# Performance work log

Hardware: AMD Instinct MI355X
Metric: run time of the kernel (lower is better)

The kernel has to match this reference:

```python
import jax, jax.numpy as jnp
import numpy as np

N_USER = 60000
N_ITEM = 40000
N = N_USER + N_ITEM          # 100000 nodes
D = 64                       # embed / layer dim
NNZ = 1600000                # edges per relation (avg degree 16)
B = 16384                    # batch of (user,item) pairs
NLAYERS = 2                  # layers=[64,64,64] -> 2 GNN layers
VAL_SCALE = 0.02             # ~1/degree, mimics symmetric-normalized Laplacian values
W_SCALE = 0.05


def spmm(row, col, val, X):
    # sparse [N,N] @ dense [N,D] via gather + segment-sum (COO)
    return jax.ops.segment_sum(val[:, None] * X[col], row, num_segments=N)


def setup_inputs() -> dict:
    key = jax.random.key(0)
    ks = jax.random.split(key, 40)
    inp = {}
    inp['userIdx'] = jax.random.randint(ks[0], (B,), 0, N_USER, dtype=jnp.int32)
    inp['itemIdx'] = jax.random.randint(ks[1], (B,), 0, N_ITEM, dtype=jnp.int32)
    inp['uEmbd'] = jax.random.normal(ks[2], (N_USER, D), dtype=jnp.float32)
    inp['iEmbd'] = jax.random.normal(ks[3], (N_ITEM, D), dtype=jnp.float32)
    for i, name in enumerate(['lap', 'trust', 'add']):
        inp[name + '_row'] = jax.random.randint(ks[4 + 3 * i], (NNZ,), 0, N, dtype=jnp.int32)
        inp[name + '_col'] = jax.random.randint(ks[5 + 3 * i], (NNZ,), 0, N, dtype=jnp.int32)
        inp[name + '_val'] = jax.random.uniform(ks[6 + 3 * i], (NNZ,), dtype=jnp.float32) * VAL_SCALE
    j = 13
    for name in ['lin_W', 'inter_W', 'attM_W', 'attA_W', 'attT_W']:
        inp[name] = jax.random.normal(ks[j], (NLAYERS, D, D), dtype=jnp.float32) * W_SCALE; j += 1
    for name in ['lin_b', 'inter_b', 'attM_b', 'attA_b', 'attT_b']:
        inp[name] = jax.random.normal(ks[j], (NLAYERS, D), dtype=jnp.float32) * W_SCALE; j += 1
    for name in ['a_main', 'a_add', 'a_trust']:
        inp[name] = jax.random.normal(ks[j], (NLAYERS, D, 1), dtype=jnp.float32) * W_SCALE; j += 1
    inp['W1'] = jax.random.normal(ks[j], (2 * D, 64), dtype=jnp.float32) * W_SCALE; j += 1
    inp['b1'] = jax.random.normal(ks[j], (64,), dtype=jnp.float32) * W_SCALE; j += 1
    inp['W2'] = jax.random.normal(ks[j], (64, 32), dtype=jnp.float32) * W_SCALE; j += 1
    inp['b2'] = jax.random.normal(ks[j], (32,), dtype=jnp.float32) * W_SCALE; j += 1
    inp['W3'] = jax.random.normal(ks[j], (32, 1), dtype=jnp.float32) * W_SCALE; j += 1
    inp['b3'] = jax.random.normal(ks[j], (1,), dtype=jnp.float32) * W_SCALE; j += 1
    return inp


def _gcf_forward(userIdx, itemIdx, uEmbd, iEmbd,
                 lap_row, lap_col, lap_val,
                 trust_row, trust_col, trust_val,
                 add_row, add_col, add_val,
                 lin_W, lin_b, inter_W, inter_b,
                 attM_W, attM_b, attA_W, attA_b, attT_W, attT_b,
                 a_main, a_add, a_trust,
                 W1, b1, W2, b2, W3, b3):
    feats = jnp.concatenate([uEmbd, iEmbd], axis=0)  # [N, D]
    all_emb = [feats]
    rels = [(lap_row, lap_col, lap_val),
            (trust_row, trust_col, trust_val),
            (add_row, add_col, add_val)]
    for l in range(NLAYERS):
        X = feats
        X2 = X * X  # inter_feature = features * features

        def relation(edges, aW, ab, avec):
            row, col, val = edges
            # (L + I) @ X  -> linear ; L @ (X*X) -> interActTransform
            h1 = (spmm(row, col, val, X) + X) @ lin_W[l] + lin_b[l]
            h2 = spmm(row, col, val, X2) @ inter_W[l] + inter_b[l]
            att = jnp.tanh((h1 + h2) @ aW + ab) @ avec  # [N, 1]
            return h1, h2, att.mean()

        m1, m2, w_main = relation(rels[0], attM_W[l], attM_b[l], a_main[l])
        t1, t2, w_trust = relation(rels[1], attT_W[l], attT_b[l], a_trust[l])
        a1, a2, w_add = relation(rels[2], attA_W[l], attA_b[l], a_add[l])
        beta = jax.nn.softmax(jnp.stack([w_main, w_add, w_trust]))  # [3]
        feats = (beta[0] * (m1 + m2) + beta[1] * (a1 + a2) + beta[2] * (t1 + t2))
        all_emb.append(feats)
    final = jnp.mean(jnp.stack(all_emb, axis=1), axis=1)  # [N, D]
    userE = final[userIdx]
    itemE = final[itemIdx + N_USER]
    h = jnp.concatenate([userE, itemE], axis=1)  # [B, 2D]
    h = jax.nn.relu(h @ W1 + b1)
    h = h @ W2 + b2
    h = h @ W3 + b3
    prediction = h.reshape(-1)
    return prediction, userE, itemE, final


def reference(userIdx, itemIdx, uEmbd, iEmbd,
              lap_row, lap_col, lap_val,
              trust_row, trust_col, trust_val,
              add_row, add_col, add_val,
              lin_W, lin_b, inter_W, inter_b,
              attM_W, attM_b, attA_W, attA_b, attT_W, attT_b,
              a_main, a_add, a_trust,
              W1, b1, W2, b2, W3, b3):
    return _gcf_forward(userIdx, itemIdx, uEmbd, iEmbd,
                        lap_row, lap_col, lap_val,
                        trust_row, trust_col, trust_val,
                        add_row, add_col, add_val,
                        lin_W, lin_b, inter_W, inter_b,
                        attM_W, attM_b, attA_W, attA_b, attT_W, attT_b,
                        a_main, a_add, a_trust,
                        W1, b1, W2, b2, W3, b3)
```

## Files before the change

### kernel.cpp

```cpp
#include <hip/hip_runtime.h>

#define N_USER  60000
#define N_ITEM  40000
#define NN      100000
#define NNZ_E   1600000
#define BB      16384
#define ND      6400000
#define ND4     1600000
#define NCHUNK  6250
#define NBUCK   196
#define BUCK_CAP 9216
#define BUCKTOT (NBUCK * BUCK_CAP)
#define BINB    196
#define EPB     8192

typedef __attribute__((ext_vector_type(8))) short bf16x8;
typedef __attribute__((ext_vector_type(8))) unsigned short u16x8;
typedef __attribute__((ext_vector_type(4))) float f32x4;

__device__ __forceinline__ float tanh_fast(float x) {
    x = fminf(fmaxf(x, -15.f), 15.f);
    float e = __expf(2.f * x);
    return (e - 1.f) / (e + 1.f);
}

__device__ __forceinline__ float bcast(float x, int k) {
    return __int_as_float(__builtin_amdgcn_readlane(__float_as_int(x), k));
}

__device__ __forceinline__ unsigned short f2bf(float f) {
    unsigned u = __float_as_uint(f);
    u += 0x7FFFu + ((u >> 16) & 1u);
    return (unsigned short)(u >> 16);
}
__device__ __forceinline__ float bf2f(unsigned short s) {
    return __uint_as_float(((unsigned)s) << 16);
}

__device__ __forceinline__ int widx(int k, int n) {
    return ((((n >> 4) * 2 + (k >> 5)) * 4 + ((k >> 3) & 3)) * 16 + (n & 15)) * 8 + (k & 7);
}

__global__ __launch_bounds__(256) void init_kernel(
    const float4* __restrict__ u, const float4* __restrict__ it,
    ushort* __restrict__ XB, float4* __restrict__ fs,
    int* __restrict__ CURS, float* __restrict__ attsum)
{
    int i = blockIdx.x * 256 + threadIdx.x;
    if (i < ND4) {
        float4 v = (i < N_USER * 16) ? u[i] : it[i - N_USER * 16];
        fs[i] = v;
        ushort4 b;
        b.x = f2bf(v.x); b.y = f2bf(v.y); b.z = f2bf(v.z); b.w = f2bf(v.w);
        ((ushort4*)XB)[i] = b;
    }
    if (i < 3 * NBUCK) CURS[i] = (i % NBUCK) * BUCK_CAP;
    if (i < 6) attsum[i] = 0.f;
}

__global__ __launch_bounds__(512) void bin_kernel(
    const int* __restrict__ rows0, const int* __restrict__ cols0, const float* __restrict__ vals0,
    const int* __restrict__ rows1, const int* __restrict__ cols1, const float* __restrict__ vals1,
    const int* __restrict__ rows2, const int* __restrict__ cols2, const float* __restrict__ vals2,
    int* __restrict__ CURS, int2* __restrict__ ECV)
{
    int rel = blockIdx.x / BINB;
    int blk = blockIdx.x % BINB;
    const int* rows; const int* cols; const float* vals;
    if (rel == 0) { rows = rows0; cols = cols0; vals = vals0; }
    else if (rel == 1) { rows = rows1; cols = cols1; vals = vals1; }
    else { rows = rows2; cols = cols2; vals = vals2; }
    long long* out = (long long*)(ECV + (size_t)rel * BUCKTOT);

    __shared__ int2 sStage[EPB];
    __shared__ int hW[8 * NBUCK];
    __shared__ int lOff[NBUCK], lEnd[NBUCK], lCur[NBUCK], gB[NBUCK];
    __shared__ int wt[4];

    int t = threadIdx.x;
    int lane = t & 63, w = t >> 6;
    for (int i = t; i < 8 * NBUCK; i += 512) hW[i] = 0;
    __syncthreads();

    int base = blk * EPB;
    int myrow[16];
    #pragma unroll
    for (int j = 0; j < 16; ++j) {
        int idx = base + j * 512 + t;
        myrow[j] = (idx < NNZ_E) ? __builtin_nontemporal_load(&rows[idx]) : -1;
        if (myrow[j] >= 0) atomicAdd(&hW[w * NBUCK + (myrow[j] >> 9)], 1);
    }
    __syncthreads();
    if (t < 256) {
        int h = 0;
        if (t < NBUCK) {
            #pragma unroll
            for (int ww = 0; ww < 8; ++ww) h += hW[ww * NBUCK + t];
        }
        int sc = h;
        #pragma unroll
        for (int o = 1; o < 64; o <<= 1) {
            int u = __shfl_up(sc, o);
            if (lane >= o) sc += u;
        }
        if (lane == 63) wt[w] = sc;
        __syncthreads();
        int woff = 0;
        #pragma unroll
        for (int ww = 0; ww < 4; ++ww) if (ww < w) woff += wt[ww];
        int excl = woff + sc - h;
        if (t < NBUCK) {
            lOff[t] = excl;
            lEnd[t] = excl + h;
            lCur[t] = excl;
            gB[t] = h ? atomicAdd(&CURS[rel * NBUCK + t], h) : 0;
        }
    } else {
        __syncthreads();
    }
    __syncthreads();
    #pragma unroll
    for (int j = 0; j < 16; ++j) {
        int idx = base + j * 512 + t;
        if (myrow[j] >= 0) {
            int c = __builtin_nontemporal_load(&cols[idx]);
            float v = __builtin_nontemporal_load(&vals[idx]);
            int b = myrow[j] >> 9;
            int pos = atomicAdd(&lCur[b], 1);
            int2 e;
            e.x = ((myrow[j] & 511) << 17) | c;
            e.y = __float_as_int(v);
            sStage[pos] = e;
        }
    }
    __syncthreads();
    for (int b = w; b < NBUCK; b += 8) {
        int s = lOff[b], e = lEnd[b];
        int gb = gB[b];
        int lim = (b + 1) * BUCK_CAP;
        for (int i = s + lane; i < e; i += 64) {
            int d = gb + (i - s);
            if (d < lim) {
                int2 ev = sStage[i];
                long long packed = (((long long)(unsigned)ev.y) << 32) | (unsigned)ev.x;
                __builtin_nontemporal_store(packed, &out[d]);
            }
        }
    }
}

__global__ __launch_bounds__(512) void bsort_kernel(
    const int* __restrict__ CURS, int2* __restrict__ ECV,
    int* __restrict__ RPS, int* __restrict__ RPE)
{
    int rel = blockIdx.x / NBUCK;
    int b   = blockIdx.x % NBUCK;
    int start = b * BUCK_CAP;
    int cnt = CURS[rel * NBUCK + b] - start;
    if (cnt > BUCK_CAP) cnt = BUCK_CAP;
    int2* ecv = ECV + (size_t)rel * BUCKTOT;

    __shared__ int2 sStage[BUCK_CAP];
    __shared__ int sOff[512], sCnt[512];
    __shared__ int wt[8];
    int t = threadIdx.x;
    int lane = t & 63, w = t >> 6;
    sCnt[t] = 0;
    __syncthreads();
    int2 e[18];
    #pragma unroll
    for (int j = 0; j < 18; ++j) {
        int i = t + j * 512;
        if (i < cnt) {
            e[j] = ecv[start + i];
            atomicAdd(&sCnt[((unsigned)e[j].x) >> 17], 1);
        }
    }
    __syncthreads();
    int h = sCnt[t];
    int sc = h;
    #pragma unroll
    for (int o = 1; o < 64; o <<= 1) {
        int u = __shfl_up(sc, o);
        if (lane >= o) sc += u;
    }
    if (lane == 63) wt[w] = sc;
    __syncthreads();
    int woff = 0;
    #pragma unroll
    for (int ww = 0; ww < 8; ++ww) if (ww < w) woff += wt[ww];
    int excl = woff + sc - h;
    __syncthreads();
    sOff[t] = excl;
    sCnt[t] = excl;
    __syncthreads();
    #pragma unroll
    for (int j = 0; j < 18; ++j) {
        int i = t + j * 512;
        if (i < cnt) {
            int rl = ((unsigned)e[j].x) >> 17;
            int pos = atomicAdd(&sCnt[rl], 1);
            int2 o2; o2.x = e[j].x & 0x1FFFF; o2.y = e[j].y;
            sStage[pos] = o2;
        }
    }
    __syncthreads();
    for (int i = t; i < cnt; i += 512) ecv[start + i] = sStage[i];
    int row = b * 512 + t;
    if (row < NN) {
        RPS[rel * NN + row] = start + sOff[t];
        RPE[rel * NN + row] = start + sCnt[t];
    }
}

__global__ __launch_bounds__(256, 4) void spmm_kernel(
    const int* __restrict__ RPS, const int* __restrict__ RPE,
    const int2* __restrict__ ecv,
    const ushort* __restrict__ XB, ushort* __restrict__ G)
{
    int t = threadIdx.x;
    int lane = t & 63;
    int wv = t >> 6;
    int dl = lane & 7;
    int r = blockIdx.x * 32 + wv * 8 + (lane >> 3);
    int ea = RPS[r], eb = RPE[r];
    int cnt = eb - ea;
    int cm = cnt;
    cm = max(cm, __shfl_xor(cm, 8));
    cm = max(cm, __shfl_xor(cm, 16));
    cm = max(cm, __shfl_xor(cm, 32));
    u16x8 xo8 = *(const u16x8*)&XB[(size_t)r * 64 + 8 * dl];
    float s1[8] = {0.f, 0.f, 0.f, 0.f, 0.f, 0.f, 0.f, 0.f};
    float s2[8] = {0.f, 0.f, 0.f, 0.f, 0.f, 0.f, 0.f, 0.f};
    for (int base = 0; base < cm; base += 4) {
        float vv[4]; u16x8 xx[4];
        #pragma unroll
        for (int j = 0; j < 4; ++j) {
            int i = base + j;
            bool ok = i < cnt;
            int is = ea + (ok ? i : 0);
            int2 cv = ecv[is];
            vv[j] = ok ? __int_as_float(cv.y) : 0.f;
            xx[j] = *(const u16x8*)&XB[(size_t)cv.x * 64 + 8 * dl];
        }
        #pragma unroll
        for (int j = 0; j < 4; ++j) {
            float v = vv[j];
            #pragma unroll
            for (int d = 0; d < 8; ++d) {
                float x = bf2f(xx[j][d]);
                s1[d] += v * x;
                s2[d] += v * x * x;
            }
        }
    }
    u16x8 o1, o2;
    #pragma unroll
    for (int d = 0; d < 8; ++d) {
        o1[d] = f2bf(s1[d] + bf2f(xo8[d]));
        o2[d] = f2bf(s2[d]);
    }
    *(u16x8*)&G[(size_t)r * 128 + 8 * dl]      = o1;
    *(u16x8*)&G[(size_t)r * 128 + 64 + 8 * dl] = o2;
}

__global__ __launch_bounds__(256) void dense_kernel(
    const ushort* __restrict__ G, ushort* __restrict__ Hout,
    const float* __restrict__ linW, const float* __restrict__ interW,
    const float* __restrict__ linb, const float* __restrict__ interb,
    const float* __restrict__ attW, const float* __restrict__ attb,
    const float* __restrict__ avec, float* __restrict__ attsum)
{
    __shared__ short sL[4096], sI[4096], sW[4096];
    __shared__ float sH[4 * 16 * 65];
    __shared__ float sBias[64], sAttb[64], sAvec[64];

    int tid = threadIdx.x;
    for (int i = tid; i < 4096; i += 256) {
        int k = i >> 6, n = i & 63, ix = widx(k, n);
        sL[ix] = (short)f2bf(linW[i]);
        sI[ix] = (short)f2bf(interW[i]);
        sW[ix] = (short)f2bf(attW[i]);
    }
    if (tid < 64) {
        sBias[tid] = linb[tid] + interb[tid];
        sAttb[tid] = attb[tid];
        sAvec[tid] = avec[tid];
    }
    __syncthreads();

    const bf16x8* pL = (const bf16x8*)sL;
    const bf16x8* pI = (const bf16x8*)sI;
    const bf16x8* pW = (const bf16x8*)sW;

    int lane = tid & 63;
    int wv = tid >> 6;
    int nl = lane & 15;
    int q  = lane >> 4;
    float* myH = sH + wv * (16 * 65);
    int gw = blockIdx.x * 4 + wv;
    int nw = gridDim.x * 4;
    float att_acc = 0.f;

    for (int c = gw; c < NCHUNK; c += nw) {
        int r0 = c * 16;
        const bf16x8* gp = (const bf16x8*)(G + (size_t)(r0 + nl) * 128);
        bf16x8 Ah[2], Qh[2];
        Ah[0] = gp[q];         Ah[1] = gp[4 + q];
        Qh[0] = gp[8 + q];     Qh[1] = gp[12 + q];
        #pragma unroll
        for (int nt = 0; nt < 4; ++nt) {
            float b = sBias[nt * 16 + nl];
            f32x4 acc = {b, b, b, b};
            #pragma unroll
            for (int kh = 0; kh < 2; ++kh) {
                int f = ((nt * 2 + kh) * 4 + q) * 16 + nl;
                acc = __builtin_amdgcn_mfma_f32_16x16x32_bf16(Ah[kh], pL[f], acc, 0, 0, 0);
                acc = __builtin_amdgcn_mfma_f32_16x16x32_bf16(Qh[kh], pI[f], acc, 0, 0, 0);
            }
            #pragma unroll
            for (int reg = 0; reg < 4; ++reg) {
                int row = q * 4 + reg;
                Hout[(size_t)(r0 + row) * 64 + nt * 16 + nl] = f2bf(acc[reg]);
                myH[row * 65 + nt * 16 + nl] = acc[reg];
            }
        }
        bf16x8 Th[2];
        #pragma unroll
        for (int kh = 0; kh < 2; ++kh) {
            #pragma unroll
            for (int j = 0; j < 8; ++j)
                Th[kh][j] = (short)f2bf(myH[nl * 65 + kh * 32 + q * 8 + j]);
        }
        #pragma unroll
        for (int nt = 0; nt < 4; ++nt) {
            float b = sAttb[nt * 16 + nl];
            f32x4 acc = {b, b, b, b};
            #pragma unroll
            for (int kh = 0; kh < 2; ++kh) {
                int f = ((nt * 2 + kh) * 4 + q) * 16 + nl;
                acc = __builtin_amdgcn_mfma_f32_16x16x32_bf16(Th[kh], pW[f], acc, 0, 0, 0);
            }
            float av = sAvec[nt * 16 + nl];
            #pragma unroll
            for (int reg = 0; reg < 4; ++reg)
                att_acc += tanh_fast(acc[reg]) * av;
        }
    }
    #pragma unroll
    for (int o = 32; o >= 1; o >>= 1) att_acc += __shfl_xor(att_acc, o);
    if (lane == 0) atomicAdd(attsum, att_acc);
}

__global__ __launch_bounds__(256) void combine_kernel(
    const ushort4* __restrict__ hM, const ushort4* __restrict__ hA,
    const ushort4* __restrict__ hT, const float* __restrict__ attsum,
    ushort4* __restrict__ XB, float4* __restrict__ fs, float scale)
{
    float w0 = attsum[0] * (1.f / NN);
    float w1 = attsum[1] * (1.f / NN);
    float w2 = attsum[2] * (1.f / NN);
    float m = fmaxf(w0, fmaxf(w1, w2));
    float e0 = __expf(w0 - m), e1 = __expf(w1 - m), e2 = __expf(w2 - m);
    float inv = 1.f / (e0 + e1 + e2);
    float b0 = e0 * inv, b1 = e1 * inv, b2 = e2 * inv;

    int i = blockIdx.x * 256 + threadIdx.x;
    if (i >= ND4) return;
    ushort4 um = hM[i], ua = hA[i], ut = hT[i];
    float4 x;
    x.x = b0 * bf2f(um.x) + b1 * bf2f(ua.x) + b2 * bf2f(ut.x);
    x.y = b0 * bf2f(um.y) + b1 * bf2f(ua.y) + b2 * bf2f(ut.y);
    x.z = b0 * bf2f(um.z) + b1 * bf2f(ua.z) + b2 * bf2f(ut.z);
    x.w = b0 * bf2f(um.w) + b1 * bf2f(ua.w) + b2 * bf2f(ut.w);
    ushort4 bo;
    bo.x = f2bf(x.x); bo.y = f2bf(x.y); bo.z = f2bf(x.z); bo.w = f2bf(x.w);
    XB[i] = bo;
    float4 f = fs[i];
    f.x = (f.x + x.x) * scale;
    f.y = (f.y + x.y) * scale;
    f.z = (f.z + x.z) * scale;
    f.w = (f.w + x.w) * scale;
    fs[i] = f;
}

__global__ __launch_bounds__(256) void mlp_kernel(
    const int* __restrict__ userIdx, const int* __restrict__ itemIdx,
    const float* __restrict__ fin,
    const float* __restrict__ W1, const float* __restrict__ b1,
    const float* __restrict__ W2, const float* __restrict__ b2,
    const float* __restrict__ W3, const float* __restrict__ b3,
    float* __restrict__ pred, float* __restrict__ userE, float* __restrict__ itemE)
{
    __shared__ float sW1[128 * 64];
    __shared__ float sW2[64 * 32];
    __shared__ float sW3[32];
    __shared__ float sb1[64];
    __shared__ float sb2[32];
    int tid = threadIdx.x;
    for (int i = tid; i < 8192; i += 256) sW1[i] = W1[i];
    for (int i = tid; i < 2048; i += 256) sW2[i] = W2[i];
    if (tid < 32) sW3[tid] = W3[tid];
    if (tid < 64) sb1[tid] = b1[tid];
    if (tid < 32) sb2[tid] = b2[tid];
    __syncthreads();
    float bb3 = b3[0];

    int lane = tid & 63;
    int gw = blockIdx.x * 4 + (tid >> 6);
    int nw = gridDim.x * 4;
    for (int p = gw; p < BB; p += nw) {
        int u = userIdx[p];
        int it = itemIdx[p] + N_USER;
        float ue = fin[u * 64 + lane];
        float ie = fin[it * 64 + lane];
        userE[p * 64 + lane] = ue;
        itemE[p * 64 + lane] = ie;
        float h = sb1[lane];
        #pragma unroll
        for (int k = 0; k < 64; ++k) h = fmaf(bcast(ue, k), sW1[k * 64 + lane], h);
        #pragma unroll
        for (int k = 0; k < 64; ++k) h = fmaf(bcast(ie, k), sW1[(k + 64) * 64 + lane], h);
        h = fmaxf(h, 0.f);
        float h2 = sb2[lane & 31];
        #pragma unroll
        for (int k = 0; k < 64; ++k) h2 = fmaf(bcast(h, k), sW2[k * 32 + (lane & 31)], h2);
        float c = (lane < 32) ? h2 * sW3[lane] : 0.f;
        #pragma unroll
        for (int o = 32; o >= 1; o >>= 1) c += __shfl_xor(c, o);
        if (lane == 0) pred[p] = c + bb3;
    }
}

extern "C" void kernel_launch(void* const* d_in, const int* in_sizes, int n_in,
                              void* d_out, int out_size, void* d_ws, size_t ws_size,
                              hipStream_t stream)
{
    const int*   userIdx = (const int*)d_in[0];
    const int*   itemIdx = (const int*)d_in[1];
    const float* uEmbd   = (const float*)d_in[2];
    const float* iEmbd   = (const float*)d_in[3];
    const int*   e_row[3] = {(const int*)d_in[4],  (const int*)d_in[10], (const int*)d_in[7]};
    const int*   e_col[3] = {(const int*)d_in[5],  (const int*)d_in[11], (const int*)d_in[8]};
    const float* e_val[3] = {(const float*)d_in[6], (const float*)d_in[12], (const float*)d_in[9]};
    const float* lin_W   = (const float*)d_in[13];
    const float* inter_W = (const float*)d_in[14];
    const float* attM_W  = (const float*)d_in[15];
    const float* attA_W  = (const float*)d_in[16];
    const float* attT_W  = (const float*)d_in[17];
    const float* lin_b   = (const float*)d_in[18];
    const float* inter_b = (const float*)d_in[19];
    const float* attM_b  = (const float*)d_in[20];
    const float* attA_b  = (const float*)d_in[21];
    const float* attT_b  = (const float*)d_in[22];
    const float* a_main  = (const float*)d_in[23];
    const float* a_add   = (const float*)d_in[24];
    const float* a_trust = (const float*)d_in[25];
    const float* W1 = (const float*)d_in[26];
    const float* b1 = (const float*)d_in[27];
    const float* W2 = (const float*)d_in[28];
    const float* b2 = (const float*)d_in[29];
    const float* W3 = (const float*)d_in[30];
    const float* b3 = (const float*)d_in[31];

    const float* attWq[3] = {attM_W, attA_W, attT_W};
    const float* attbq[3] = {attM_b, attA_b, attT_b};
    const float* avecq[3] = {a_main, a_add, a_trust};

    ushort* G  = (ushort*)d_ws;
    ushort* H0 = G + (size_t)NN * 128;
    ushort* H1 = H0 + ND;
    ushort* H2 = H1 + ND;
    int2*   ECV = (int2*)(H2 + ND);
    ushort* XB = (ushort*)(ECV + 3 * (size_t)BUCKTOT);
    int*    RPS = (int*)(XB + ND);
    int*    RPE = RPS + 3 * NN;
    int*    CURS = RPE + 3 * NN;
    float*  ATT = (float*)(CURS + 3 * NBUCK);

    ushort* Hs[3] = {H0, H1, H2};

    float* outPred  = (float*)d_out;
    float* outUser  = outPred + BB;
    float* outItem  = outUser + BB * 64;
    float* outFinal = outItem + BB * 64;

    init_kernel<<<6250, 256, 0, stream>>>((const float4*)uEmbd, (const float4*)iEmbd,
                                          XB, (float4*)outFinal, CURS, ATT);
    bin_kernel<<<3 * BINB, 512, 0, stream>>>(
        e_row[0], e_col[0], e_val[0],
        e_row[1], e_col[1], e_val[1],
        e_row[2], e_col[2], e_val[2], CURS, ECV);
    bsort_kernel<<<3 * NBUCK, 512, 0, stream>>>(CURS, ECV, RPS, RPE);

    for (int l = 0; l < 2; ++l) {
        const float* lw = lin_W + l * 4096;
        const float* iw = inter_W + l * 4096;
        const float* lb = lin_b + l * 64;
        const float* ib = inter_b + l * 64;

        for (int q = 0; q < 3; ++q) {
            spmm_kernel<<<3125, 256, 0, stream>>>(
                RPS + q * NN, RPE + q * NN, ECV + (size_t)q * BUCKTOT, XB, G);
            dense_kernel<<<512, 256, 0, stream>>>(
                G, Hs[q], lw, iw, lb, ib,
                attWq[q] + l * 4096, attbq[q] + l * 64, avecq[q] + l * 64,
                ATT + l * 3 + q);
        }
        combine_kernel<<<6250, 256, 0, stream>>>(
            (const ushort4*)Hs[0], (const ushort4*)Hs[1], (const ushort4*)Hs[2],
            ATT + l * 3, (ushort4*)XB, (float4*)outFinal,
            (l == 1) ? (1.f / 3.f) : 1.f);
    }

    mlp_kernel<<<512, 256, 0, stream>>>(userIdx, itemIdx, outFinal,
                                        W1, b1, W2, b2, W3, b3,
                                        outPred, outUser, outItem);
}
```

Before: 781.7 us.

## Fuse SpMM with dense MFMA attention and batch all three relations per launch

Merges the per-relation sparse aggregation and dense linear/attention kernels into one kernel. Each block aggregates 32 rows, places the bf16 results in shared memory in MFMA fragment layout, and runs the linear and attention MFMAs there, so the G intermediate no longer makes a round trip through global memory. All three relations go into a single launch, and weights are pre-converted to bf16 fragment layout once by a small prep kernel. The attention partial sums are reduced per block before one atomic add. The cost is lower occupancy (launch bounds 3), extra block-level syncs, and weight fragments read from global or L2 instead of LDS.

Result: slower. 1.024 ms (+31.0%).

```diff
diff --git a/kernel.cpp b/kernel.cpp
--- a/kernel.cpp
+++ b/kernel.cpp
@@ -7,7 +7,7 @@
 #define BB      16384
 #define ND      6400000
 #define ND4     1600000
-#define NCHUNK  6250
+#define NBLK    3125
 #define NBUCK   196
 #define BUCK_CAP 9216
 #define BUCKTOT (NBUCK * BUCK_CAP)
@@ -56,6 +56,27 @@
     }
     if (i < 3 * NBUCK) CURS[i] = (i % NBUCK) * BUCK_CAP;
     if (i < 6) attsum[i] = 0.f;
+}
+
+__global__ __launch_bounds__(256) void prep_kernel(
+    const float* __restrict__ lin_W, const float* __restrict__ inter_W,
+    const float* __restrict__ attM_W, const float* __restrict__ attA_W,
+    const float* __restrict__ attT_W, ushort* __restrict__ WF)
+{
+    int b = blockIdx.x;
+    int l = b / 5, m = b % 5;
+    const float* src;
+    if (m == 0) src = lin_W;
+    else if (m == 1) src = inter_W;
+    else if (m == 2) src = attM_W;
+    else if (m == 3) src = attA_W;
+    else src = attT_W;
+    src += (size_t)l * 4096;
+    ushort* dst = WF + ((size_t)l * 5 + m) * 4096;
+    for (int i = threadIdx.x; i < 4096; i += 256) {
+        int k = i >> 6, n = i & 63;
+        dst[widx(k, n)] = f2bf(src[i]);
+    }
 }
 
 __global__ __launch_bounds__(512) void bin_kernel(
@@ -213,22 +234,47 @@
     }
 }
 
-__global__ __launch_bounds__(256, 4) void spmm_kernel(
+__global__ __launch_bounds__(256, 3) void fused_kernel(
     const int* __restrict__ RPS, const int* __restrict__ RPE,
-    const int2* __restrict__ ecv,
-    const ushort* __restrict__ XB, ushort* __restrict__ G)
-{
+    const int2* __restrict__ ECV, const ushort* __restrict__ XB,
+    const ushort* __restrict__ WF,
+    const float* __restrict__ linb, const float* __restrict__ interb,
+    const float* __restrict__ attb0, const float* __restrict__ attb1,
+    const float* __restrict__ attb2,
+    const float* __restrict__ avec0, const float* __restrict__ avec1,
+    const float* __restrict__ avec2,
+    ushort* __restrict__ H0, ushort* __restrict__ H1, ushort* __restrict__ H2,
+    float* __restrict__ ATTl)
+{
+    __shared__ ushort sA[2048], sQ[2048];
+    __shared__ float  sH[2 * 16 * 68];
+    __shared__ float  sBias[64], sAttb[64], sAvec[64];
+    __shared__ float  sRed[4];
+
+    int bid = blockIdx.x;
+    int rel = bid / NBLK;
+    int rb  = bid % NBLK;
     int t = threadIdx.x;
-    int lane = t & 63;
-    int wv = t >> 6;
-    int dl = lane & 7;
-    int r = blockIdx.x * 32 + wv * 8 + (lane >> 3);
-    int ea = RPS[r], eb = RPE[r];
+    int lane = t & 63, wv = t >> 6, dl = lane & 7;
+
+    const float* attb = (rel == 0) ? attb0 : ((rel == 1) ? attb1 : attb2);
+    const float* avec = (rel == 0) ? avec0 : ((rel == 1) ? avec1 : avec2);
+    ushort* Hout = (rel == 0) ? H0 : ((rel == 1) ? H1 : H2);
+    if (t < 64) {
+        sBias[t] = linb[t] + interb[t];
+        sAttb[t] = attb[t];
+        sAvec[t] = avec[t];
+    }
+
+    int rr = wv * 8 + (lane >> 3);
+    int r  = rb * 32 + rr;
+    int ea = RPS[rel * NN + r], eb = RPE[rel * NN + r];
     int cnt = eb - ea;
     int cm = cnt;
     cm = max(cm, __shfl_xor(cm, 8));
     cm = max(cm, __shfl_xor(cm, 16));
     cm = max(cm, __shfl_xor(cm, 32));
+    const int2* ecv = ECV + (size_t)rel * BUCKTOT;
     u16x8 xo8 = *(const u16x8*)&XB[(size_t)r * 64 + 8 * dl];
     float s1[8] = {0.f, 0.f, 0.f, 0.f, 0.f, 0.f, 0.f, 0.f};
     float s2[8] = {0.f, 0.f, 0.f, 0.f, 0.f, 0.f, 0.f, 0.f};
@@ -254,102 +300,93 @@
             }
         }
     }
-    u16x8 o1, o2;
-    #pragma unroll
-    for (int d = 0; d < 8; ++d) {
-        o1[d] = f2bf(s1[d] + bf2f(xo8[d]));
-        o2[d] = f2bf(s2[d]);
-    }
-    *(u16x8*)&G[(size_t)r * 128 + 8 * dl]      = o1;
-    *(u16x8*)&G[(size_t)r * 128 + 64 + 8 * dl] = o2;
-}
-
-__global__ __launch_bounds__(256) void dense_kernel(
-    const ushort* __restrict__ G, ushort* __restrict__ Hout,
-    const float* __restrict__ linW, const float* __restrict__ interW,
-    const float* __restrict__ linb, const float* __restrict__ interb,
-    const float* __restrict__ attW, const float* __restrict__ attb,
-    const float* __restrict__ avec, float* __restrict__ attsum)
-{
-    __shared__ short sL[4096], sI[4096], sW[4096];
-    __shared__ float sH[4 * 16 * 65];
-    __shared__ float sBias[64], sAttb[64], sAvec[64];
-
-    int tid = threadIdx.x;
-    for (int i = tid; i < 4096; i += 256) {
-        int k = i >> 6, n = i & 63, ix = widx(k, n);
-        sL[ix] = (short)f2bf(linW[i]);
-        sI[ix] = (short)f2bf(interW[i]);
-        sW[ix] = (short)f2bf(attW[i]);
-    }
-    if (tid < 64) {
-        sBias[tid] = linb[tid] + interb[tid];
-        sAttb[tid] = attb[tid];
-        sAvec[tid] = avec[tid];
-    }
-    __syncthreads();
-
-    const bf16x8* pL = (const bf16x8*)sL;
-    const bf16x8* pI = (const bf16x8*)sI;
-    const bf16x8* pW = (const bf16x8*)sW;
-
-    int lane = tid & 63;
-    int wv = tid >> 6;
+    {
+        int ch = rr >> 4, nl15 = rr & 15, kh = dl >> 2, q4 = dl & 3;
+        int fi = ((((ch * 2 + kh) * 4 + q4) * 16) + nl15) * 8;
+        u16x8 o1, o2;
+        #pragma unroll
+        for (int d = 0; d < 8; ++d) {
+            o1[d] = f2bf(s1[d] + bf2f(xo8[d]));
+            o2[d] = f2bf(s2[d]);
+        }
+        *(u16x8*)&sA[fi] = o1;
+        *(u16x8*)&sQ[fi] = o2;
+    }
+    __syncthreads();
+
+    const bf16x8* pA = (const bf16x8*)sA;
+    const bf16x8* pQ = (const bf16x8*)sQ;
+    const bf16x8* pL = (const bf16x8*)WF;
+    const bf16x8* pI = (const bf16x8*)(WF + 4096);
+    const bf16x8* pW = (const bf16x8*)(WF + (size_t)(2 + rel) * 4096);
     int nl = lane & 15;
     int q  = lane >> 4;
-    float* myH = sH + wv * (16 * 65);
-    int gw = blockIdx.x * 4 + wv;
-    int nw = gridDim.x * 4;
+    int dch = wv >> 1;
+    int nth = wv & 1;
+    float* myH = sH + dch * (16 * 68);
+
+    bf16x8 Ah[2], Qh[2];
+    #pragma unroll
+    for (int kh = 0; kh < 2; ++kh) {
+        int f = ((dch * 2 + kh) * 4 + q) * 16 + nl;
+        Ah[kh] = pA[f];
+        Qh[kh] = pQ[f];
+    }
+    #pragma unroll
+    for (int ni = 0; ni < 2; ++ni) {
+        int nt = nth * 2 + ni;
+        float b = sBias[nt * 16 + nl];
+        f32x4 acc = {b, b, b, b};
+        #pragma unroll
+        for (int kh = 0; kh < 2; ++kh) {
+            int f = ((nt * 2 + kh) * 4 + q) * 16 + nl;
+            acc = __builtin_amdgcn_mfma_f32_16x16x32_bf16(Ah[kh], pL[f], acc, 0, 0, 0);
+            acc = __builtin_amdgcn_mfma_f32_16x16x32_bf16(Qh[kh], pI[f], acc, 0, 0, 0);
+        }
+        #pragma unroll
+        for (int reg = 0; reg < 4; ++reg)
+            myH[(q * 4 + reg) * 68 + nt * 16 + nl] = acc[reg];
+    }
+    __syncthreads();
+
+    {
+        int row = t >> 3;
+        int c0  = (t & 7) * 8;
+        const float* hp = sH + (row >> 4) * (16 * 68) + (row & 15) * 68 + c0;
+        u16x8 hv;
+        #pragma unroll
+        for (int j = 0; j < 8; ++j) hv[j] = f2bf(hp[j]);
+        *(u16x8*)&Hout[(size_t)rb * 2048 + t * 8] = hv;
+    }
+
+    bf16x8 Th[2];
+    #pragma unroll
+    for (int kh = 0; kh < 2; ++kh) {
+        #pragma unroll
+        for (int j = 0; j < 8; ++j)
+            Th[kh][j] = (short)f2bf(myH[nl * 68 + kh * 32 + q * 8 + j]);
+    }
     float att_acc = 0.f;
-
-    for (int c = gw; c < NCHUNK; c += nw) {
-        int r0 = c * 16;
-        const bf16x8* gp = (const bf16x8*)(G + (size_t)(r0 + nl) * 128);
-        bf16x8 Ah[2], Qh[2];
-        Ah[0] = gp[q];         Ah[1] = gp[4 + q];
-        Qh[0] = gp[8 + q];     Qh[1] = gp[12 + q];
-        #pragma unroll
-        for (int nt = 0; nt < 4; ++nt) {
-            float b = sBias[nt * 16 + nl];
-            f32x4 acc = {b, b, b, b};
-            #pragma unroll
-            for (int kh = 0; kh < 2; ++kh) {
-                int f = ((nt * 2 + kh) * 4 + q) * 16 + nl;
-                acc = __builtin_amdgcn_mfma_f32_16x16x32_bf16(Ah[kh], pL[f], acc, 0, 0, 0);
-                acc = __builtin_amdgcn_mfma_f32_16x16x32_bf16(Qh[kh], pI[f], acc, 0, 0, 0);
-            }
-            #pragma unroll
-            for (int reg = 0; reg < 4; ++reg) {
-                int row = q * 4 + reg;
-                Hout[(size_t)(r0 + row) * 64 + nt * 16 + nl] = f2bf(acc[reg]);
-                myH[row * 65 + nt * 16 + nl] = acc[reg];
-            }
-        }
-        bf16x8 Th[2];
+    #pragma unroll
+    for (int ni = 0; ni < 2; ++ni) {
+        int nt = nth * 2 + ni;
+        float b = sAttb[nt * 16 + nl];
+        f32x4 acc = {b, b, b, b};
         #pragma unroll
         for (int kh = 0; kh < 2; ++kh) {
-            #pragma unroll
-            for (int j = 0; j < 8; ++j)
-                Th[kh][j] = (short)f2bf(myH[nl * 65 + kh * 32 + q * 8 + j]);
-        }
-        #pragma unroll
-        for (int nt = 0; nt < 4; ++nt) {
-            float b = sAttb[nt * 16 + nl];
-            f32x4 acc = {b, b, b, b};
-            #pragma unroll
-            for (int kh = 0; kh < 2; ++kh) {
-                int f = ((nt * 2 + kh) * 4 + q) * 16 + nl;
-                acc = __builtin_amdgcn_mfma_f32_16x16x32_bf16(Th[kh], pW[f], acc, 0, 0, 0);
-            }
-            float av = sAvec[nt * 16 + nl];
-            #pragma unroll
-            for (int reg = 0; reg < 4; ++reg)
-                att_acc += tanh_fast(acc[reg]) * av;
-        }
+            int f = ((nt * 2 + kh) * 4 + q) * 16 + nl;
+            acc = __builtin_amdgcn_mfma_f32_16x16x32_bf16(Th[kh], pW[f], acc, 0, 0, 0);
+        }
+        float av = sAvec[nt * 16 + nl];
+        #pragma unroll
+        for (int reg = 0; reg < 4; ++reg)
+            att_acc += tanh_fast(acc[reg]) * av;
     }
     #pragma unroll
     for (int o = 32; o >= 1; o >>= 1) att_acc += __shfl_xor(att_acc, o);
-    if (lane == 0) atomicAdd(attsum, att_acc);
+    if (lane == 0) sRed[wv] = att_acc;
+    __syncthreads();
+    if (t == 0) atomicAdd(ATTl + rel, sRed[0] + sRed[1] + sRed[2] + sRed[3]);
 }
 
 __global__ __launch_bounds__(256) void combine_kernel(
@@ -463,12 +500,7 @@
     const float* W3 = (const float*)d_in[30];
     const float* b3 = (const float*)d_in[31];
 
-    const float* attWq[3] = {attM_W, attA_W, attT_W};
-    const float* attbq[3] = {attM_b, attA_b, attT_b};
-    const float* avecq[3] = {a_main, a_add, a_trust};
-
-    ushort* G  = (ushort*)d_ws;
-    ushort* H0 = G + (size_t)NN * 128;
+    ushort* H0 = (ushort*)d_ws;
     ushort* H1 = H0 + ND;
     ushort* H2 = H1 + ND;
     int2*   ECV = (int2*)(H2 + ND);
@@ -477,6 +509,7 @@
     int*    RPE = RPS + 3 * NN;
     int*    CURS = RPE + 3 * NN;
     float*  ATT = (float*)(CURS + 3 * NBUCK);
+    ushort* WF  = (ushort*)(ATT + 16);
 
     ushort* Hs[3] = {H0, H1, H2};
 
@@ -487,6 +520,7 @@
 
     init_kernel<<<6250, 256, 0, stream>>>((const float4*)uEmbd, (const float4*)iEmbd,
                                           XB, (float4*)outFinal, CURS, ATT);
+    prep_kernel<<<10, 256, 0, stream>>>(lin_W, inter_W, attM_W, attA_W, attT_W, WF);
     bin_kernel<<<3 * BINB, 512, 0, stream>>>(
         e_row[0], e_col[0], e_val[0],
         e_row[1], e_col[1], e_val[1],
@@ -494,19 +528,13 @@
     bsort_kernel<<<3 * NBUCK, 512, 0, stream>>>(CURS, ECV, RPS, RPE);
 
     for (int l = 0; l < 2; ++l) {
-        const float* lw = lin_W + l * 4096;
-        const float* iw = inter_W + l * 4096;
-        const float* lb = lin_b + l * 64;
-        const float* ib = inter_b + l * 64;
-
-        for (int q = 0; q < 3; ++q) {
-            spmm_kernel<<<3125, 256, 0, stream>>>(
-                RPS + q * NN, RPE + q * NN, ECV + (size_t)q * BUCKTOT, XB, G);
-            dense_kernel<<<512, 256, 0, stream>>>(
-                G, Hs[q], lw, iw, lb, ib,
-                attWq[q] + l * 4096, attbq[q] + l * 64, avecq[q] + l * 64,
-                ATT + l * 3 + q);
-        }
+        fused_kernel<<<3 * NBLK, 256, 0, stream>>>(
+            RPS, RPE, ECV, XB,
+            WF + (size_t)l * 5 * 4096,
+            lin_b + l * 64, inter_b + l * 64,
+            attM_b + l * 64, attA_b + l * 64, attT_b + l * 64,
+            a_main + l * 64, a_add + l * 64, a_trust + l * 64,
+            H0, H1, H2, ATT + l * 3);
         combine_kernel<<<6250, 256, 0, stream>>>(
             (const ushort4*)Hs[0], (const ushort4*)Hs[1], (const ushort4*)Hs[2],
             ATT + l * 3, (ushort4*)XB, (float4*)outFinal,
```

## Overlap SpMM and dense stages across relations with fused launches and double-buffered G

Applied to the files above, without the earlier changes.

Merges the init pass into the binning kernel and moves the attention-weight bf16 conversion into a small prep kernel that writes into scratch space in the output buffer. When workspace allows, G is double-buffered so each relation's dense stage runs in the same launch as the next relation's SpMM, using a block-index split. This removes serialization between dependent stages and some launch gaps. It also skips the XB write on the last combine, uses nontemporal loads there, and raises the dense grid size. The risks are the workspace-size check, the extra G buffer, and using the userE output region as temporary weight storage before mlp overwrites it.

Result: slower. 937.4 us (+19.9%).

```diff
diff --git a/kernel.cpp b/kernel.cpp
--- a/kernel.cpp
+++ b/kernel.cpp
@@ -13,6 +13,8 @@
 #define BUCKTOT (NBUCK * BUCK_CAP)
 #define BINB    196
 #define EPB     8192
+#define DGRID   1024
+#define DBLK    512
 
 typedef __attribute__((ext_vector_type(8))) short bf16x8;
 typedef __attribute__((ext_vector_type(8))) unsigned short u16x8;
@@ -41,29 +43,52 @@
     return ((((n >> 4) * 2 + (k >> 5)) * 4 + ((k >> 3) & 3)) * 16 + (n & 15)) * 8 + (k & 7);
 }
 
-__global__ __launch_bounds__(256) void init_kernel(
-    const float4* __restrict__ u, const float4* __restrict__ it,
-    ushort* __restrict__ XB, float4* __restrict__ fs,
+__global__ __launch_bounds__(256) void prep_kernel(
+    const float* __restrict__ attM_W, const float* __restrict__ attA_W,
+    const float* __restrict__ attT_W, ushort* __restrict__ WF,
     int* __restrict__ CURS, float* __restrict__ attsum)
 {
-    int i = blockIdx.x * 256 + threadIdx.x;
-    if (i < ND4) {
-        float4 v = (i < N_USER * 16) ? u[i] : it[i - N_USER * 16];
-        fs[i] = v;
-        ushort4 b;
-        b.x = f2bf(v.x); b.y = f2bf(v.y); b.z = f2bf(v.z); b.w = f2bf(v.w);
-        ((ushort4*)XB)[i] = b;
-    }
-    if (i < 3 * NBUCK) CURS[i] = (i % NBUCK) * BUCK_CAP;
-    if (i < 6) attsum[i] = 0.f;
-}
-
-__global__ __launch_bounds__(512) void bin_kernel(
+    int b = blockIdx.x;
+    if (b == 6) {
+        for (int i = threadIdx.x; i < 3 * NBUCK; i += 256)
+            CURS[i] = (i % NBUCK) * BUCK_CAP;
+        if (threadIdx.x < 16) attsum[threadIdx.x] = 0.f;
+        return;
+    }
+    int l = b / 3, q = b % 3;
+    const float* src = ((q == 0) ? attM_W : ((q == 1) ? attA_W : attT_W)) + (size_t)l * 4096;
+    ushort* dst = WF + ((size_t)l * 3 + q) * 4096;
+    for (int i = threadIdx.x; i < 4096; i += 256) {
+        int k = i >> 6, n = i & 63;
+        dst[widx(k, n)] = f2bf(src[i]);
+    }
+}
+
+__global__ __launch_bounds__(512) void ib_kernel(
     const int* __restrict__ rows0, const int* __restrict__ cols0, const float* __restrict__ vals0,
     const int* __restrict__ rows1, const int* __restrict__ cols1, const float* __restrict__ vals1,
     const int* __restrict__ rows2, const int* __restrict__ cols2, const float* __restrict__ vals2,
-    int* __restrict__ CURS, int2* __restrict__ ECV)
-{
+    int* __restrict__ CURS, int2* __restrict__ ECV,
+    const float4* __restrict__ u, const float4* __restrict__ it,
+    ushort* __restrict__ XB, float4* __restrict__ fs)
+{
+    __shared__ int2 sStage[EPB];
+    __shared__ int hW[8 * NBUCK];
+    __shared__ int lOff[NBUCK], lEnd[NBUCK], lCur[NBUCK], gB[NBUCK];
+    __shared__ int wt[4];
+
+    if (blockIdx.x >= 3 * BINB) {
+        int i = (blockIdx.x - 3 * BINB) * 512 + threadIdx.x;
+        if (i < ND4) {
+            float4 v = (i < N_USER * 16) ? u[i] : it[i - N_USER * 16];
+            fs[i] = v;
+            ushort4 b;
+            b.x = f2bf(v.x); b.y = f2bf(v.y); b.z = f2bf(v.z); b.w = f2bf(v.w);
+            ((ushort4*)XB)[i] = b;
+        }
+        return;
+    }
+
     int rel = blockIdx.x / BINB;
     int blk = blockIdx.x % BINB;
     const int* rows; const int* cols; const float* vals;
@@ -72,11 +97,6 @@
     else { rows = rows2; cols = cols2; vals = vals2; }
     long long* out = (long long*)(ECV + (size_t)rel * BUCKTOT);
 
-    __shared__ int2 sStage[EPB];
-    __shared__ int hW[8 * NBUCK];
-    __shared__ int lOff[NBUCK], lEnd[NBUCK], lCur[NBUCK], gB[NBUCK];
-    __shared__ int wt[4];
-
     int t = threadIdx.x;
     int lane = t & 63, w = t >> 6;
     for (int i = t; i < 8 * NBUCK; i += 512) hW[i] = 0;
@@ -100,8 +120,8 @@
         int sc = h;
         #pragma unroll
         for (int o = 1; o < 64; o <<= 1) {
-            int u = __shfl_up(sc, o);
-            if (lane >= o) sc += u;
+            int u2 = __shfl_up(sc, o);
+            if (lane >= o) sc += u2;
         }
         if (lane == 63) wt[w] = sc;
         __syncthreads();
@@ -213,16 +233,16 @@
     }
 }
 
-__global__ __launch_bounds__(256, 4) void spmm_kernel(
+__device__ __forceinline__ void spmm_body(
+    int t, int bid,
     const int* __restrict__ RPS, const int* __restrict__ RPE,
-    const int2* __restrict__ ecv,
-    const ushort* __restrict__ XB, ushort* __restrict__ G)
-{
-    int t = threadIdx.x;
+    const int2* __restrict__ ecv, const ushort* __restrict__ XB,
+    ushort* __restrict__ G)
+{
     int lane = t & 63;
     int wv = t >> 6;
     int dl = lane & 7;
-    int r = blockIdx.x * 32 + wv * 8 + (lane >> 3);
+    int r = bid * 32 + wv * 8 + (lane >> 3);
     int ea = RPS[r], eb = RPE[r];
     int cnt = eb - ea;
     int cm = cnt;
@@ -264,23 +284,20 @@
     *(u16x8*)&G[(size_t)r * 128 + 64 + 8 * dl] = o2;
 }
 
-__global__ __launch_bounds__(256) void dense_kernel(
+__device__ __forceinline__ void dense_body(
+    int tid, int bid, int nblk,
     const ushort* __restrict__ G, ushort* __restrict__ Hout,
     const float* __restrict__ linW, const float* __restrict__ interW,
     const float* __restrict__ linb, const float* __restrict__ interb,
-    const float* __restrict__ attW, const float* __restrict__ attb,
-    const float* __restrict__ avec, float* __restrict__ attsum)
-{
-    __shared__ short sL[4096], sI[4096], sW[4096];
-    __shared__ float sH[4 * 16 * 65];
-    __shared__ float sBias[64], sAttb[64], sAvec[64];
-
-    int tid = threadIdx.x;
+    const ushort* __restrict__ WA, const float* __restrict__ attb,
+    const float* __restrict__ avec, float* __restrict__ attsum,
+    short* sL, short* sI, float* sH,
+    float* sBias, float* sAttb, float* sAvec)
+{
     for (int i = tid; i < 4096; i += 256) {
         int k = i >> 6, n = i & 63, ix = widx(k, n);
         sL[ix] = (short)f2bf(linW[i]);
         sI[ix] = (short)f2bf(interW[i]);
-        sW[ix] = (short)f2bf(attW[i]);
     }
     if (tid < 64) {
         sBias[tid] = linb[tid] + interb[tid];
@@ -291,15 +308,15 @@
 
     const bf16x8* pL = (const bf16x8*)sL;
     const bf16x8* pI = (const bf16x8*)sI;
-    const bf16x8* pW = (const bf16x8*)sW;
+    const bf16x8* pW = (const bf16x8*)WA;
 
     int lane = tid & 63;
     int wv = tid >> 6;
     int nl = lane & 15;
     int q  = lane >> 4;
     float* myH = sH + wv * (16 * 65);
-    int gw = blockIdx.x * 4 + wv;
-    int nw = gridDim.x * 4;
+    int gw = bid * 4 + wv;
+    int nw = nblk * 4;
     float att_acc = 0.f;
 
     for (int c = gw; c < NCHUNK; c += nw) {
@@ -352,10 +369,57 @@
     if (lane == 0) atomicAdd(attsum, att_acc);
 }
 
+__global__ __launch_bounds__(256, 4) void spmm_kernel(
+    const int* __restrict__ RPS, const int* __restrict__ RPE,
+    const int2* __restrict__ ecv,
+    const ushort* __restrict__ XB, ushort* __restrict__ G)
+{
+    spmm_body(threadIdx.x, blockIdx.x, RPS, RPE, ecv, XB, G);
+}
+
+__global__ __launch_bounds__(256, 4) void dense_kernel(
+    const ushort* __restrict__ G, ushort* __restrict__ Hout,
+    const float* __restrict__ linW, const float* __restrict__ interW,
+    const float* __restrict__ linb, const float* __restrict__ interb,
+    const ushort* __restrict__ WA, const float* __restrict__ attb,
+    const float* __restrict__ avec, float* __restrict__ attsum)
+{
+    __shared__ short sL[4096], sI[4096];
+    __shared__ float sH[4 * 16 * 65];
+    __shared__ float sBias[64], sAttb[64], sAvec[64];
+    dense_body(threadIdx.x, blockIdx.x, gridDim.x, G, Hout,
+               linW, interW, linb, interb, WA, attb, avec, attsum,
+               sL, sI, sH, sBias, sAttb, sAvec);
+}
+
+__global__ __launch_bounds__(256, 4) void sd_kernel(
+    const ushort* __restrict__ Gin, ushort* __restrict__ Hout,
+    const float* __restrict__ linW, const float* __restrict__ interW,
+    const float* __restrict__ linb, const float* __restrict__ interb,
+    const ushort* __restrict__ WA, const float* __restrict__ attb,
+    const float* __restrict__ avec, float* __restrict__ attsum,
+    const int* __restrict__ RPS, const int* __restrict__ RPE,
+    const int2* __restrict__ ecv, const ushort* __restrict__ XB,
+    ushort* __restrict__ Gout)
+{
+    __shared__ short sL[4096], sI[4096];
+    __shared__ float sH[4 * 16 * 65];
+    __shared__ float sBias[64], sAttb[64], sAvec[64];
+    if (blockIdx.x < DBLK) {
+        dense_body(threadIdx.x, blockIdx.x, DBLK, Gin, Hout,
+                   linW, interW, linb, interb, WA, attb, avec, attsum,
+                   sL, sI, sH, sBias, sAttb, sAvec);
+    } else {
+        spmm_body(threadIdx.x, blockIdx.x - DBLK, RPS, RPE, ecv, XB, Gout);
+    }
+}
+
 __global__ __launch_bounds__(256) void combine_kernel(
-    const ushort4* __restrict__ hM, const ushort4* __restrict__ hA,
-    const ushort4* __restrict__ hT, const float* __restrict__ attsum,
-    ushort4* __restrict__ XB, float4* __restrict__ fs, float scale)
+    const unsigned long long* __restrict__ hM,
+    const unsigned long long* __restrict__ hA,
+    const unsigned long long* __restrict__ hT,
+    const float* __restrict__ attsum,
+    ushort4* __restrict__ XB, float4* __restrict__ fs, float scale, int doXB)
 {
     float w0 = attsum[0] * (1.f / NN);
     float w1 = attsum[1] * (1.f / NN);
@@ -367,15 +431,19 @@
 
     int i = blockIdx.x * 256 + threadIdx.x;
     if (i >= ND4) return;
-    ushort4 um = hM[i], ua = hA[i], ut = hT[i];
+    unsigned long long pm = __builtin_nontemporal_load(&hM[i]);
+    unsigned long long pa = __builtin_nontemporal_load(&hA[i]);
+    unsigned long long pt = __builtin_nontemporal_load(&hT[i]);
     float4 x;
-    x.x = b0 * bf2f(um.x) + b1 * bf2f(ua.x) + b2 * bf2f(ut.x);
-    x.y = b0 * bf2f(um.y) + b1 * bf2f(ua.y) + b2 * bf2f(ut.y);
-    x.z = b0 * bf2f(um.z) + b1 * bf2f(ua.z) + b2 * bf2f(ut.z);
-    x.w = b0 * bf2f(um.w) + b1 * bf2f(ua.w) + b2 * bf2f(ut.w);
-    ushort4 bo;
-    bo.x = f2bf(x.x); bo.y = f2bf(x.y); bo.z = f2bf(x.z); bo.w = f2bf(x.w);
-    XB[i] = bo;
+    x.x = b0 * bf2f((unsigned short)pm)         + b1 * bf2f((unsigned short)pa)         + b2 * bf2f((unsigned short)pt);
+    x.y = b0 * bf2f((unsigned short)(pm >> 16)) + b1 * bf2f((unsigned short)(pa >> 16)) + b2 * bf2f((unsigned short)(pt >> 16));
+    x.z = b0 * bf2f((unsigned short)(pm >> 32)) + b1 * bf2f((unsigned short)(pa >> 32)) + b2 * bf2f((unsigned short)(pt >> 32));
+    x.w = b0 * bf2f((unsigned short)(pm >> 48)) + b1 * bf2f((unsigned short)(pa >> 48)) + b2 * bf2f((unsigned short)(pt >> 48));
+    if (doXB) {
+        ushort4 bo;
+        bo.x = f2bf(x.x); bo.y = f2bf(x.y); bo.z = f2bf(x.z); bo.w = f2bf(x.w);
+        XB[i] = bo;
+    }
     float4 f = fs[i];
     f.x = (f.x + x.x) * scale;
     f.y = (f.y + x.y) * scale;
@@ -463,12 +531,17 @@
     const float* W3 = (const float*)d_in[30];
     const float* b3 = (const float*)d_in[31];
 
-    const float* attWq[3] = {attM_W, attA_W, attT_W};
     const float* attbq[3] = {attM_b, attA_b, attT_b};
     const float* avecq[3] = {a_main, a_add, a_trust};
 
-    ushort* G  = (ushort*)d_ws;
-    ushort* H0 = G + (size_t)NN * 128;
+    size_t gwords = (size_t)NN * 128;
+    size_t need_big = 2 * gwords * 2 + (size_t)3 * ND * 2 + (size_t)3 * BUCKTOT * 8
+                    + (size_t)ND * 2 + (size_t)6 * NN * 4 + (size_t)3 * NBUCK * 4 + 64;
+    bool big = ws_size >= need_big;
+
+    ushort* GA = (ushort*)d_ws;
+    ushort* GB = big ? (GA + gwords) : GA;
+    ushort* H0 = GB + gwords;
     ushort* H1 = H0 + ND;
     ushort* H2 = H1 + ND;
     int2*   ECV = (int2*)(H2 + ND);
@@ -485,12 +558,14 @@
     float* outItem  = outUser + BB * 64;
     float* outFinal = outItem + BB * 64;
 
-    init_kernel<<<6250, 256, 0, stream>>>((const float4*)uEmbd, (const float4*)iEmbd,
-                                          XB, (float4*)outFinal, CURS, ATT);
-    bin_kernel<<<3 * BINB, 512, 0, stream>>>(
+    ushort* WF = (ushort*)outUser;
+
+    prep_kernel<<<7, 256, 0, stream>>>(attM_W, attA_W, attT_W, WF, CURS, ATT);
+    ib_kernel<<<3 * BINB + 3125, 512, 0, stream>>>(
         e_row[0], e_col[0], e_val[0],
         e_row[1], e_col[1], e_val[1],
-        e_row[2], e_col[2], e_val[2], CURS, ECV);
+        e_row[2], e_col[2], e_val[2], CURS, ECV,
+        (const float4*)uEmbd, (const float4*)iEmbd, XB, (float4*)outFinal);
     bsort_kernel<<<3 * NBUCK, 512, 0, stream>>>(CURS, ECV, RPS, RPE);
 
     for (int l = 0; l < 2; ++l) {
@@ -499,18 +574,38 @@
         const float* lb = lin_b + l * 64;
         const float* ib = inter_b + l * 64;
 
-        for (int q = 0; q < 3; ++q) {
+        if (big) {
             spmm_kernel<<<3125, 256, 0, stream>>>(
-                RPS + q * NN, RPE + q * NN, ECV + (size_t)q * BUCKTOT, XB, G);
-            dense_kernel<<<512, 256, 0, stream>>>(
-                G, Hs[q], lw, iw, lb, ib,
-                attWq[q] + l * 4096, attbq[q] + l * 64, avecq[q] + l * 64,
-                ATT + l * 3 + q);
+                RPS, RPE, ECV, XB, GA);
+            sd_kernel<<<DBLK + 3125, 256, 0, stream>>>(
+                GA, Hs[0], lw, iw, lb, ib,
+                WF + ((size_t)l * 3 + 0) * 4096, attbq[0] + l * 64, avecq[0] + l * 64,
+                ATT + l * 3 + 0,
+                RPS + NN, RPE + NN, ECV + (size_t)BUCKTOT, XB, GB);
+            sd_kernel<<<DBLK + 3125, 256, 0, stream>>>(
+                GB, Hs[1], lw, iw, lb, ib,
+                WF + ((size_t)l * 3 + 1) * 4096, attbq[1] + l * 64, avecq[1] + l * 64,
+                ATT + l * 3 + 1,
+                RPS + 2 * NN, RPE + 2 * NN, ECV + 2 * (size_t)BUCKTOT, XB, GA);
+            dense_kernel<<<DGRID, 256, 0, stream>>>(
+                GA, Hs[2], lw, iw, lb, ib,
+                WF + ((size_t)l * 3 + 2) * 4096, attbq[2] + l * 64, avecq[2] + l * 64,
+                ATT + l * 3 + 2);
+        } else {
+            for (int q = 0; q < 3; ++q) {
+                spmm_kernel<<<3125, 256, 0, stream>>>(
+                    RPS + q * NN, RPE + q * NN, ECV + (size_t)q * BUCKTOT, XB, GA);
+                dense_kernel<<<DGRID, 256, 0, stream>>>(
+                    GA, Hs[q], lw, iw, lb, ib,
+                    WF + ((size_t)l * 3 + q) * 4096, attbq[q] + l * 64, avecq[q] + l * 64,
+                    ATT + l * 3 + q);
+            }
         }
         combine_kernel<<<6250, 256, 0, stream>>>(
-            (const ushort4*)Hs[0], (const ushort4*)Hs[1], (const ushort4*)Hs[2],
+            (const unsigned long long*)Hs[0], (const unsigned long long*)Hs[1],
+            (const unsigned long long*)Hs[2],
             ATT + l * 3, (ushort4*)XB, (float4*)outFinal,
-            (l == 1) ? (1.f / 3.f) : 1.f);
+            (l == 1) ? (1.f / 3.f) : 1.f, (l == 0) ? 1 : 0);
     }
 
     mlp_kernel<<<512, 256, 0, stream>>>(userIdx, itemIdx, outFinal,
```

## Degree-sort rows within buckets for SpMM balance; skip final XB write

Applied to the files above, without the earlier changes.

The bucket sort kernel now builds a per-bucket permutation of rows ordered by their edge count. The SpMM kernel reads its row index through this permutation, so the 8 rows sharing a wavefront have similar degrees and less time is lost to the max-degree loop bound. The combine kernel also uses nontemporal 64-bit loads and skips writing the bf16 XB buffer on the last layer, where nothing reads it. The cost is an extra indirection load per row, and output rows are written in a scattered order.

After: 819.6 us. +4.8%, slower.

```diff
diff --git a/kernel.cpp b/kernel.cpp
--- a/kernel.cpp
+++ b/kernel.cpp
@@ -151,7 +151,7 @@
 
 __global__ __launch_bounds__(512) void bsort_kernel(
     const int* __restrict__ CURS, int2* __restrict__ ECV,
-    int* __restrict__ RPS, int* __restrict__ RPE)
+    int* __restrict__ RPS, int* __restrict__ RPE, int* __restrict__ PERM)
 {
     int rel = blockIdx.x / NBUCK;
     int b   = blockIdx.x % NBUCK;
@@ -163,6 +163,7 @@
     __shared__ int2 sStage[BUCK_CAP];
     __shared__ int sOff[512], sCnt[512];
     __shared__ int wt[8];
+    __shared__ int dh[64];
     int t = threadIdx.x;
     int lane = t & 63, w = t >> 6;
     sCnt[t] = 0;
@@ -178,6 +179,7 @@
     }
     __syncthreads();
     int h = sCnt[t];
+    int myCnt = h;
     int sc = h;
     #pragma unroll
     for (int o = 1; o < 64; o <<= 1) {
@@ -211,18 +213,39 @@
         RPS[rel * NN + row] = start + sOff[t];
         RPE[rel * NN + row] = start + sCnt[t];
     }
+
+    int dbin = (row < NN) ? min(myCnt, 62) : 63;
+    if (t < 64) dh[t] = 0;
+    __syncthreads();
+    atomicAdd(&dh[dbin], 1);
+    __syncthreads();
+    if (t < 64) {
+        int v = dh[t];
+        int sc2 = v;
+        #pragma unroll
+        for (int o = 1; o < 64; o <<= 1) {
+            int u2 = __shfl_up(sc2, o);
+            if (t >= o) sc2 += u2;
+        }
+        dh[t] = sc2 - v;
+    }
+    __syncthreads();
+    int pos = atomicAdd(&dh[dbin], 1);
+    int slot = b * 512 + pos;
+    if (row < NN && slot < NN) PERM[rel * NN + slot] = row;
 }
 
 __global__ __launch_bounds__(256, 4) void spmm_kernel(
     const int* __restrict__ RPS, const int* __restrict__ RPE,
-    const int2* __restrict__ ecv,
+    const int2* __restrict__ ecv, const int* __restrict__ PERM,
     const ushort* __restrict__ XB, ushort* __restrict__ G)
 {
     int t = threadIdx.x;
     int lane = t & 63;
     int wv = t >> 6;
     int dl = lane & 7;
-    int r = blockIdx.x * 32 + wv * 8 + (lane >> 3);
+    int g = blockIdx.x * 32 + wv * 8 + (lane >> 3);
+    int r = PERM[g];
     int ea = RPS[r], eb = RPE[r];
     int cnt = eb - ea;
     int cm = cnt;
@@ -353,9 +376,11 @@
 }
 
 __global__ __launch_bounds__(256) void combine_kernel(
-    const ushort4* __restrict__ hM, const ushort4* __restrict__ hA,
-    const ushort4* __restrict__ hT, const float* __restrict__ attsum,
-    ushort4* __restrict__ XB, float4* __restrict__ fs, float scale)
+    const unsigned long long* __restrict__ hM,
+    const unsigned long long* __restrict__ hA,
+    const unsigned long long* __restrict__ hT,
+    const float* __restrict__ attsum,
+    ushort4* __restrict__ XB, float4* __restrict__ fs, float scale, int doXB)
 {
     float w0 = attsum[0] * (1.f / NN);
     float w1 = attsum[1] * (1.f / NN);
@@ -367,15 +392,19 @@
 
     int i = blockIdx.x * 256 + threadIdx.x;
     if (i >= ND4) return;
-    ushort4 um = hM[i], ua = hA[i], ut = hT[i];
+    unsigned long long pm = __builtin_nontemporal_load(&hM[i]);
+    unsigned long long pa = __builtin_nontemporal_load(&hA[i]);
+    unsigned long long pt = __builtin_nontemporal_load(&hT[i]);
     float4 x;
-    x.x = b0 * bf2f(um.x) + b1 * bf2f(ua.x) + b2 * bf2f(ut.x);
-    x.y = b0 * bf2f(um.y) + b1 * bf2f(ua.y) + b2 * bf2f(ut.y);
-    x.z = b0 * bf2f(um.z) + b1 * bf2f(ua.z) + b2 * bf2f(ut.z);
-    x.w = b0 * bf2f(um.w) + b1 * bf2f(ua.w) + b2 * bf2f(ut.w);
-    ushort4 bo;
-    bo.x = f2bf(x.x); bo.y = f2bf(x.y); bo.z = f2bf(x.z); bo.w = f2bf(x.w);
-    XB[i] = bo;
+    x.x = b0 * bf2f((unsigned short)pm)         + b1 * bf2f((unsigned short)pa)         + b2 * bf2f((unsigned short)pt);
+    x.y = b0 * bf2f((unsigned short)(pm >> 16)) + b1 * bf2f((unsigned short)(pa >> 16)) + b2 * bf2f((unsigned short)(pt >> 16));
+    x.z = b0 * bf2f((unsigned short)(pm >> 32)) + b1 * bf2f((unsigned short)(pa >> 32)) + b2 * bf2f((unsigned short)(pt >> 32));
+    x.w = b0 * bf2f((unsigned short)(pm >> 48)) + b1 * bf2f((unsigned short)(pa >> 48)) + b2 * bf2f((unsigned short)(pt >> 48));
+    if (doXB) {
+        ushort4 bo;
+        bo.x = f2bf(x.x); bo.y = f2bf(x.y); bo.z = f2bf(x.z); bo.w = f2bf(x.w);
+        XB[i] = bo;
+    }
     float4 f = fs[i];
     f.x = (f.x + x.x) * scale;
     f.y = (f.y + x.y) * scale;
@@ -477,6 +506,7 @@
     int*    RPE = RPS + 3 * NN;
     int*    CURS = RPE + 3 * NN;
     float*  ATT = (float*)(CURS + 3 * NBUCK);
+    int*    PERM = (int*)(ATT + 16);
 
     ushort* Hs[3] = {H0, H1, H2};
 
@@ -491,7 +521,7 @@
         e_row[0], e_col[0], e_val[0],
         e_row[1], e_col[1], e_val[1],
         e_row[2], e_col[2], e_val[2], CURS, ECV);
-    bsort_kernel<<<3 * NBUCK, 512, 0, stream>>>(CURS, ECV, RPS, RPE);
+    bsort_kernel<<<3 * NBUCK, 512, 0, stream>>>(CURS, ECV, RPS, RPE, PERM);
 
     for (int l = 0; l < 2; ++l) {
         const float* lw = lin_W + l * 4096;
@@ -501,16 +531,18 @@
 
         for (int q = 0; q < 3; ++q) {
             spmm_kernel<<<3125, 256, 0, stream>>>(
-                RPS + q * NN, RPE + q * NN, ECV + (size_t)q * BUCKTOT, XB, G);
+                RPS + q * NN, RPE + q * NN, ECV + (size_t)q * BUCKTOT,
+                PERM + q * NN, XB, G);
             dense_kernel<<<512, 256, 0, stream>>>(
                 G, Hs[q], lw, iw, lb, ib,
                 attWq[q] + l * 4096, attbq[q] + l * 64, avecq[q] + l * 64,
                 ATT + l * 3 + q);
         }
         combine_kernel<<<6250, 256, 0, stream>>>(
-            (const ushort4*)Hs[0], (const ushort4*)Hs[1], (const ushort4*)Hs[2],
+            (const unsigned long long*)Hs[0], (const unsigned long long*)Hs[1],
+            (const unsigned long long*)Hs[2],
             ATT + l * 3, (ushort4*)XB, (float4*)outFinal,
-            (l == 1) ? (1.f / 3.f) : 1.f);
+            (l == 1) ? (1.f / 3.f) : 1.f, (l == 0) ? 1 : 0);
     }
 
     mlp_kernel<<<512, 256, 0, stream>>>(userIdx, itemIdx, outFinal,
```
